# Kernel optimization log

Hardware: AMD Instinct MI355X
Metric: run time of the kernel (lower is better)

## Reference

```python
import jax, jax.numpy as jnp
import numpy as np

B, GRID, CIN, COUT, TDIM, NMODES = 32, 128, 32, 32, 256, 32
M = NMODES // 2 + 1  # kept modes per axis = 17
FFT_NORM = 'forward'


def setup_inputs() -> dict:
    key = jax.random.key(0)
    ks = jax.random.split(key, 10)
    w_std = float(np.sqrt(1.0 / (2.0 * CIN)))          # normal_initializer(in_co_dim)
    k_std = float(np.sqrt(1.0 / TDIM))                 # ~lecun_normal for Dense kernels
    wshape = (M, M, CIN, COUT)
    return {
        'x': jax.random.normal(ks[0], (B, GRID, GRID, CIN), jnp.float32),
        't_emb': jax.random.normal(ks[1], (B, TDIM), jnp.float32),
        'w1_real': w_std * jax.random.normal(ks[2], wshape, jnp.float32),
        'w1_imag': w_std * jax.random.normal(ks[3], wshape, jnp.float32),
        'w2_real': w_std * jax.random.normal(ks[4], wshape, jnp.float32),
        'w2_imag': w_std * jax.random.normal(ks[5], wshape, jnp.float32),
        'k1_real': k_std * jax.random.normal(ks[6], (TDIM, M), jnp.float32),
        'k1_imag': k_std * jax.random.normal(ks[7], (TDIM, M), jnp.float32),
        'k2_real': k_std * jax.random.normal(ks[8], (TDIM, M), jnp.float32),
        'k2_imag': k_std * jax.random.normal(ks[9], (TDIM, M), jnp.float32),
    }


def reference(x, t_emb, w1_real, w1_imag, w2_real, w2_imag,
              k1_real, k1_imag, k2_real, k2_imag):
    b, n = x.shape[0], x.shape[1]
    # rFFT2 over spatial axes: (b, n, n//2+1, cin) complex
    x_ft = jnp.fft.rfft2(x, axes=(1, 2), norm=FFT_NORM)

    w1 = w1_real + 1j * w1_imag  # (M, M, cin, cout)
    w2 = w2_real + 1j * w2_imag
    # Time modulation: Dense(no bias) -> complex per-mode scale t[b, i].
    # The original builds diag(t) and einsums it into the weights; that equals a
    # simple broadcast scale over the first mode axis, fused here.
    t1 = (t_emb @ k1_real) + 1j * (t_emb @ k1_imag)  # (b, M)
    t2 = (t_emb @ k2_real) + 1j * (t_emb @ k2_imag)

    # Mode-truncated complex channel contraction, scaled by t along axis i.
    xf1 = jnp.einsum('bijc,ijco->bijo', x_ft[:, :M, :M, :], w1) * t1[:, :, None, None]
    xf2 = jnp.einsum('bijc,ijco->bijo', x_ft[:, -M:, :M, :], w2) * t2[:, :, None, None]

    out_ft = jnp.zeros((b, n, n // 2 + 1, COUT), dtype=jnp.complex64)
    out_ft = out_ft.at[:, :M, :M, :].set(xf1)
    out_ft = out_ft.at[:, -M:, :M, :].set(xf2)

    return jnp.fft.irfft2(out_ft, s=(n, n), axes=(1, 2), norm=FFT_NORM)
```

## Files before the change

kernel.cpp:

```cpp
#include <hip/hip_runtime.h>
#include <stdint.h>


#define TWO_PI_OVER_128 0.04908738521234052f

__global__ __launch_bounds__(128) void k_tproj(
    const float* __restrict__ temb, const float* __restrict__ k1r, const float* __restrict__ k1i,
    const float* __restrict__ k2r, const float* __restrict__ k2i, float* __restrict__ tbuf)
{
    int b = blockIdx.x, tid = threadIdx.x;
    __shared__ float ts[256];
    for (int d = tid; d < 256; d += 128) ts[d] = temb[b * 256 + d];
    __syncthreads();
    if (tid < 68) {
        int which = (tid >= 34) ? 1 : 0;
        int rem = tid - which * 34;
        int i = rem >> 1, part = rem & 1;
        const float* kp = which ? (part ? k2i : k2r) : (part ? k1i : k1r);
        float a0 = 0.f, a1 = 0.f, a2 = 0.f, a3 = 0.f;
        for (int d = 0; d < 256; d += 4) {
            a0 = fmaf(ts[d],     kp[(d)     * 17 + i], a0);
            a1 = fmaf(ts[d + 1], kp[(d + 1) * 17 + i], a1);
            a2 = fmaf(ts[d + 2], kp[(d + 2) * 17 + i], a2);
            a3 = fmaf(ts[d + 3], kp[(d + 3) * 17 + i], a3);
        }
        tbuf[((which * 32 + b) * 17 + i) * 2 + part] = (a0 + a1) + (a2 + a3);
    }
}

__global__ __launch_bounds__(64) void k_fwd_y(const float* __restrict__ x, float2* __restrict__ T1)
{
    int blk = blockIdx.x;
    int b = blk >> 7, xr = blk & 127;
    __shared__ float xs[128 * 32];
    __shared__ float2 cst[128];
    int tid = threadIdx.x;
    {
        float s0, c0; sincosf(TWO_PI_OVER_128 * (float)tid, &s0, &c0);
        cst[tid] = make_float2(c0, -s0);
        float s1, c1; sincosf(TWO_PI_OVER_128 * (float)(tid + 64), &s1, &c1);
        cst[tid + 64] = make_float2(c1, -s1);
    }
    const float4* xv = (const float4*)(x + ((size_t)blk << 12));
    float4* xs4 = (float4*)xs;
#pragma unroll
    for (int i = 0; i < 16; ++i) xs4[tid + (i << 6)] = xv[tid + (i << 6)];
    __syncthreads();
    for (int i = tid; i < 2016; i += 64) {
        int y = (i >> 5) + 1, c = i & 31;
        float a = xs[(y << 5) + c], q = xs[((128 - y) << 5) + c];
        xs[(y << 5) + c] = a + q;
        xs[((128 - y) << 5) + c] = a - q;
    }
    __syncthreads();
    int jg = tid >> 3, cg = tid & 7, c0 = cg << 2;
    float re[2][4] = {{0,0,0,0},{0,0,0,0}}, im[2][4] = {{0,0,0,0},{0,0,0,0}};
    int j0 = jg, j1 = jg + 8;
    int idx0 = 0, idx1 = 0;
    for (int y = 1; y <= 63; ++y) {
        idx0 = (idx0 + j0) & 127;
        idx1 = (idx1 + j1) & 127;
        float2 w0 = cst[idx0], w1 = cst[idx1];
        float4 s = *(const float4*)&xs[(y << 5) + c0];
        float4 d = *(const float4*)&xs[((128 - y) << 5) + c0];
        re[0][0] = fmaf(s.x, w0.x, re[0][0]);
        re[0][1] = fmaf(s.y, w0.x, re[0][1]);
        re[0][2] = fmaf(s.z, w0.x, re[0][2]);
        re[0][3] = fmaf(s.w, w0.x, re[0][3]);
        im[0][0] = fmaf(d.x, w0.y, im[0][0]);
        im[0][1] = fmaf(d.y, w0.y, im[0][1]);
        im[0][2] = fmaf(d.z, w0.y, im[0][2]);
        im[0][3] = fmaf(d.w, w0.y, im[0][3]);
        re[1][0] = fmaf(s.x, w1.x, re[1][0]);
        re[1][1] = fmaf(s.y, w1.x, re[1][1]);
        re[1][2] = fmaf(s.z, w1.x, re[1][2]);
        re[1][3] = fmaf(s.w, w1.x, re[1][3]);
        im[1][0] = fmaf(d.x, w1.y, im[1][0]);
        im[1][1] = fmaf(d.y, w1.y, im[1][1]);
        im[1][2] = fmaf(d.z, w1.y, im[1][2]);
        im[1][3] = fmaf(d.w, w1.y, im[1][3]);
    }
    const float s_ = 1.f / 16384.f;
    float x0[4], x64[4];
    *(float4*)x0  = *(const float4*)&xs[c0];
    *(float4*)x64 = *(const float4*)&xs[(64 << 5) + c0];
#pragma unroll
    for (int t = 0; t < 2; ++t) {
        int j = jg + t * 8;
        float sg = (j & 1) ? -1.f : 1.f;
        float2* p = T1 + (((size_t)(b * 17 + j) * 128 + xr) << 5) + c0;
        float4 v0 = make_float4((re[t][0] + x0[0] + sg * x64[0]) * s_, im[t][0] * s_,
                                (re[t][1] + x0[1] + sg * x64[1]) * s_, im[t][1] * s_);
        float4 v1 = make_float4((re[t][2] + x0[2] + sg * x64[2]) * s_, im[t][2] * s_,
                                (re[t][3] + x0[3] + sg * x64[3]) * s_, im[t][3] * s_);
        ((float4*)p)[0] = v0; ((float4*)p)[1] = v1;
    }
    {
        float re2[4] = {0,0,0,0}, im2[4] = {0,0,0,0};
        float2 w16 = cst[(16 * (jg + 1)) & 127];
        for (int y = jg + 1; y <= 63; y += 8) {
            float4 s = *(const float4*)&xs[(y << 5) + c0];
            float4 d = *(const float4*)&xs[((128 - y) << 5) + c0];
            re2[0] = fmaf(s.x, w16.x, re2[0]); re2[1] = fmaf(s.y, w16.x, re2[1]);
            re2[2] = fmaf(s.z, w16.x, re2[2]); re2[3] = fmaf(s.w, w16.x, re2[3]);
            im2[0] = fmaf(d.x, w16.y, im2[0]); im2[1] = fmaf(d.y, w16.y, im2[1]);
            im2[2] = fmaf(d.z, w16.y, im2[2]); im2[3] = fmaf(d.w, w16.y, im2[3]);
        }
#pragma unroll
        for (int t = 0; t < 4; ++t) {
            re2[t] += __shfl_xor(re2[t], 8);
            re2[t] += __shfl_xor(re2[t], 16);
            re2[t] += __shfl_xor(re2[t], 32);
            im2[t] += __shfl_xor(im2[t], 8);
            im2[t] += __shfl_xor(im2[t], 16);
            im2[t] += __shfl_xor(im2[t], 32);
        }
        if (jg == 0) {
            float2* p = T1 + (((size_t)(b * 17 + 16) * 128 + xr) << 5) + c0;
            float4 v0 = make_float4((re2[0] + x0[0] + x64[0]) * s_, im2[0] * s_,
                                    (re2[1] + x0[1] + x64[1]) * s_, im2[1] * s_);
            float4 v1 = make_float4((re2[2] + x0[2] + x64[2]) * s_, im2[2] * s_,
                                    (re2[3] + x0[3] + x64[3]) * s_, im2[3] * s_);
            ((float4*)p)[0] = v0; ((float4*)p)[1] = v1;
        }
    }
}

#define XFS 34
__global__ __launch_bounds__(512) void k_mid_fused(
    const float2* __restrict__ T1, const float* __restrict__ w1r, const float* __restrict__ w1i,
    const float* __restrict__ w2r, const float* __restrict__ w2i,
    const float* __restrict__ tbuf, float2* __restrict__ U)
{
    int blk = blockIdx.x;
    int b = blk / 17, j = blk - b * 17;
    __shared__ float4 Ts4[2048];
    __shared__ float2 Xf[34 * XFS];
    __shared__ float2 cst[128];
    int tid = threadIdx.x;
    const float4* s4 = (const float4*)(T1 + (size_t)blk * 4096);
    for (int i = tid; i < 2048; i += 512) Ts4[i] = s4[i];
    if (tid < 128) {
        float s, c; sincosf(TWO_PI_OVER_128 * (float)tid, &s, &c);
        cst[tid] = make_float2(c, s);
    }
    __syncthreads();
    for (int i = tid; i < 1008; i += 512) {
        int xx = (i >> 4) + 1, cp = i & 15;
        float4 a = Ts4[(xx << 4) + cp], q = Ts4[((128 - xx) << 4) + cp];
        Ts4[(xx << 4) + cp] = make_float4(a.x + q.x, a.y + q.y, a.z + q.z, a.w + q.w);
        Ts4[((128 - xx) << 4) + cp] = make_float4(a.x - q.x, a.y - q.y, a.z - q.z, a.w - q.w);
    }
    __syncthreads();
    if (tid < 288) {
        int cp = tid & 15, u = tid >> 4;
        float4 t0 = Ts4[cp], t64 = Ts4[(64 << 4) + cp];
        if (u < 16) {
            int f = u + 1;
            int idx = 0;
            float P0=0,Q0=0,R0=0,T0=0,P1=0,Q1=0,R1=0,T1a=0;
            for (int xx = 1; xx <= 63; ++xx) {
                idx = (idx + f) & 127;
                float2 w = cst[idx];
                float4 S = Ts4[(xx << 4) + cp];
                float4 D = Ts4[((128 - xx) << 4) + cp];
                P0 = fmaf(S.x, w.x, P0); Q0 = fmaf(D.y, w.y, Q0);
                R0 = fmaf(S.y, w.x, R0); T0 = fmaf(D.x, w.y, T0);
                P1 = fmaf(S.z, w.x, P1); Q1 = fmaf(D.w, w.y, Q1);
                R1 = fmaf(S.w, w.x, R1); T1a = fmaf(D.z, w.y, T1a);
            }
            float sg = (f & 1) ? -1.f : 1.f;
            float b0r = t0.x + sg * t64.x, b0i = t0.y + sg * t64.y;
            float b1r = t0.z + sg * t64.z, b1i = t0.w + sg * t64.w;
            int ia = f, ib = 34 - f;
            Xf[ia * XFS + cp*2]   = make_float2(P0 + Q0 + b0r, R0 - T0 + b0i);
            Xf[ia * XFS + cp*2+1] = make_float2(P1 + Q1 + b1r, R1 - T1a + b1i);
            Xf[ib * XFS + cp*2]   = make_float2(P0 - Q0 + b0r, R0 + T0 + b0i);
            Xf[ib * XFS + cp*2+1] = make_float2(P1 - Q1 + b1r, R1 + T1a + b1i);
        } else if (u == 16) {
            float A0=0,B0=0,A1=0,B1=0;
            for (int xx = 1; xx <= 63; ++xx) {
                float4 S = Ts4[(xx << 4) + cp];
                A0 += S.x; B0 += S.y; A1 += S.z; B1 += S.w;
            }
            Xf[cp*2]   = make_float2(A0 + t0.x + t64.x, B0 + t0.y + t64.y);
            Xf[cp*2+1] = make_float2(A1 + t0.z + t64.z, B1 + t0.w + t64.w);
        } else {
            int idx = 0;
            float p0=0,q0=0,r0=0,s0=0,p1=0,q1=0,r1=0,s1=0;
            for (int xx = 1; xx <= 63; ++xx) {
                idx = (idx + 111) & 127;
                float2 w = cst[idx];
                float4 S = Ts4[(xx << 4) + cp];
                float4 D = Ts4[((128 - xx) << 4) + cp];
                p0 = fmaf(S.x, w.x, p0); q0 = fmaf(D.y, w.y, q0);
                r0 = fmaf(S.y, w.x, r0); s0 = fmaf(D.x, w.y, s0);
                p1 = fmaf(S.z, w.x, p1); q1 = fmaf(D.w, w.y, q1);
                r1 = fmaf(S.w, w.x, r1); s1 = fmaf(D.z, w.y, s1);
            }
            float c0r = t0.x - t64.x, c0i = t0.y - t64.y;
            float c1r = t0.z - t64.z, c1i = t0.w - t64.w;
            Xf[17*XFS + cp*2]   = make_float2(p0 + q0 + c0r, r0 - s0 + c0i);
            Xf[17*XFS + cp*2+1] = make_float2(p1 + q1 + c1r, r1 - s1 + c1i);
        }
    }
    __syncthreads();
    float2* Ys = (float2*)Ts4;
    if (tid < 272) {
        int oq = tid & 7, ii = tid >> 3;
        int o0 = oq << 2;
        int irow = (ii < 17) ? ii : ii - 17;
        const float* wr = ((ii < 17) ? w1r : w2r) + ((irow * 17 + j) << 10) + o0;
        const float* wi = ((ii < 17) ? w1i : w2i) + ((irow * 17 + j) << 10) + o0;
        float ar0=0,ai0=0,ar1=0,ai1=0,ar2=0,ai2=0,ar3=0,ai3=0;
#pragma unroll 4
        for (int c = 0; c < 32; ++c) {
            float2 xv = Xf[ii * XFS + c];
            float4 wre = *(const float4*)(wr + (c << 5));
            float4 wim = *(const float4*)(wi + (c << 5));
            ar0 = fmaf(xv.x, wre.x, ar0); ar0 = fmaf(-xv.y, wim.x, ar0);
            ai0 = fmaf(xv.x, wim.x, ai0); ai0 = fmaf( xv.y, wre.x, ai0);
            ar1 = fmaf(xv.x, wre.y, ar1); ar1 = fmaf(-xv.y, wim.y, ar1);
            ai1 = fmaf(xv.x, wim.y, ai1); ai1 = fmaf( xv.y, wre.y, ai1);
            ar2 = fmaf(xv.x, wre.z, ar2); ar2 = fmaf(-xv.y, wim.z, ar2);
            ai2 = fmaf(xv.x, wim.z, ai2); ai2 = fmaf( xv.y, wre.z, ai2);
            ar3 = fmaf(xv.x, wre.w, ar3); ar3 = fmaf(-xv.y, wim.w, ar3);
            ai3 = fmaf(xv.x, wim.w, ai3); ai3 = fmaf( xv.y, wre.w, ai3);
        }
        int which = (ii >= 17) ? 1 : 0;
        const float* tp = tbuf + ((which * 32 + b) * 17 + irow) * 2;
        float tr = tp[0], ti = tp[1];
        float2* yp = Ys + ii * 32 + o0;
        float4 y01 = make_float4(ar0 * tr - ai0 * ti, ar0 * ti + ai0 * tr,
                                 ar1 * tr - ai1 * ti, ar1 * ti + ai1 * tr);
        float4 y23 = make_float4(ar2 * tr - ai2 * ti, ar2 * ti + ai2 * tr,
                                 ar3 * tr - ai3 * ti, ar3 * ti + ai3 * tr);
        ((float4*)yp)[0] = y01;
        ((float4*)yp)[1] = y23;
    }
    __syncthreads();
    {
        int o = tid & 31, g = tid >> 5;
        float yr[34], yi[34];
#pragma unroll
        for (int i = 0; i < 34; ++i) { float2 v = Ys[i * 32 + o]; yr[i] = v.x; yi[i] = v.y; }
        float2* Ub = U + ((size_t)b * 128 * 17 + j) * 32 + o;
        if (g == 0) {
            float sr = 0.f, si = 0.f;
#pragma unroll
            for (int i = 0; i < 34; ++i) { sr += yr[i]; si += yi[i]; }
            Ub[0] = make_float2(sr, si);
        }
        if (g == 1) {
            float sr = 0.f, si = 0.f;
#pragma unroll
            for (int i = 0; i < 34; ++i) {
                float sg2 = (i & 1) ? -1.f : 1.f;
                sr = fmaf(sg2, yr[i], sr); si = fmaf(sg2, yi[i], si);
            }
            Ub[(size_t)64 * 544] = make_float2(sr, si);
        }
        for (int k = 0; k < 2; ++k) {
            int x = 1 + g + (k << 4);
            float A1e=0,A1o=0,A2e=0,A2o=0,A3e=0,A3o=0,A4e=0,A4o=0;
            int idx = 0;
#pragma unroll
            for (int i = 0; i < 17; ++i) {
                float2 w = cst[idx];
                if (i & 1) {
                    A1o = fmaf(yr[i], w.x, A1o); A4o = fmaf(yr[i], w.y, A4o);
                    A3o = fmaf(yi[i], w.x, A3o); A2o = fmaf(yi[i], w.y, A2o);
                } else {
                    A1e = fmaf(yr[i], w.x, A1e); A4e = fmaf(yr[i], w.y, A4e);
                    A3e = fmaf(yi[i], w.x, A3e); A2e = fmaf(yi[i], w.y, A2e);
                }
                idx = (idx + x) & 127;
            }
            idx = (111 * x) & 127;
#pragma unroll
            for (int i = 17; i < 34; ++i) {
                float2 w = cst[idx];
                if (i & 1) {
                    A1o = fmaf(yr[i], w.x, A1o); A4o = fmaf(yr[i], w.y, A4o);
                    A3o = fmaf(yi[i], w.x, A3o); A2o = fmaf(yi[i], w.y, A2o);
                } else {
                    A1e = fmaf(yr[i], w.x, A1e); A4e = fmaf(yr[i], w.y, A4e);
                    A3e = fmaf(yi[i], w.x, A3e); A2e = fmaf(yi[i], w.y, A2e);
                }
                idx = (idx + x) & 127;
            }
            float A1 = A1e + A1o, A2 = A2e + A2o, A3 = A3e + A3o, A4 = A4e + A4o;
            float E1 = A1e - A1o, E2 = A2o - A2e, E3 = A3e - A3o, E4 = A4o - A4e;
            Ub[(size_t)x * 544]         = make_float2(A1 - A2, A3 + A4);
            Ub[(size_t)(128 - x) * 544] = make_float2(A1 + A2, A3 - A4);
            Ub[(size_t)(64 - x) * 544]  = make_float2(E1 - E2, E3 + E4);
            Ub[(size_t)(64 + x) * 544]  = make_float2(E1 + E2, E3 - E4);
        }
    }
}

__global__ __launch_bounds__(256) void k_fwd_x_mix(
    const float2* __restrict__ T1, const float* __restrict__ w1r, const float* __restrict__ w1i,
    const float* __restrict__ w2r, const float* __restrict__ w2i,
    const float* __restrict__ tbuf, float2* __restrict__ Y)
{
    int blk = blockIdx.x;
    int b = blk / 17, j = blk - b * 17;
    __shared__ float4 Ts4[2048];
    __shared__ float2 Xf[34 * 32];
    int tid = threadIdx.x;
    const float4* s4 = (const float4*)(T1 + (size_t)blk * 4096);
    for (int i = tid; i < 2048; i += 256) Ts4[i] = s4[i];
    __syncthreads();
    {
        int cp = tid & 15, g = tid >> 4;
        int il[3] = {g, g + 16, g + 32};
        float stc[3], sts[3];
#pragma unroll
        for (int t = 0; t < 3; ++t) {
            int i = il[t];
            int f = (i < 17) ? i : i + 94;
            float a = -TWO_PI_OVER_128 * (float)(f & 127);
            sincosf(a, &sts[t], &stc[t]);
        }
        float cr[3] = {1.f, 1.f, 1.f}, ci[3] = {0.f, 0.f, 0.f};
        float r0[3] = {0,0,0}, i0[3] = {0,0,0}, r1[3] = {0,0,0}, i1[3] = {0,0,0};
        const float4* Tc = Ts4 + cp;
#pragma unroll 2
        for (int xx = 0; xx < 128; ++xx) {
            float4 tv = Tc[xx << 4];
#pragma unroll
            for (int t = 0; t < 3; ++t) {
                r0[t] += tv.x * cr[t] - tv.y * ci[t];
                i0[t] += tv.x * ci[t] + tv.y * cr[t];
                r1[t] += tv.z * cr[t] - tv.w * ci[t];
                i1[t] += tv.z * ci[t] + tv.w * cr[t];
                float nr = cr[t] * stc[t] - ci[t] * sts[t];
                ci[t] = fmaf(cr[t], sts[t], ci[t] * stc[t]);
                cr[t] = nr;
            }
        }
#pragma unroll
        for (int t = 0; t < 3; ++t) {
            int i = il[t];
            if (i < 34) {
                Xf[i * 32 + cp * 2]     = make_float2(r0[t], i0[t]);
                Xf[i * 32 + cp * 2 + 1] = make_float2(r1[t], i1[t]);
            }
        }
    }
    __syncthreads();
    {
        int o = tid & 31, gi = tid >> 5;
#pragma unroll
        for (int t = 0; t < 5; ++t) {
            int ii = gi + (t << 3);
            if (ii < 34) {
                int irow = (ii < 17) ? ii : ii - 17;
                const float* wr = ((ii < 17) ? w1r : w2r) + ((irow * 17 + j) << 10) + o;
                const float* wi = ((ii < 17) ? w1i : w2i) + ((irow * 17 + j) << 10) + o;
                float ar = 0.f, ai = 0.f;
#pragma unroll 8
                for (int cc2 = 0; cc2 < 32; ++cc2) {
                    float2 xv = Xf[ii * 32 + cc2];
                    float wre = wr[cc2 << 5];
                    float wim = wi[cc2 << 5];
                    ar += xv.x * wre - xv.y * wim;
                    ai += xv.x * wim + xv.y * wre;
                }
                int which = (ii >= 17) ? 1 : 0;
                const float* tp = tbuf + ((which * 32 + b) * 17 + irow) * 2;
                float tr = tp[0], ti = tp[1];
                Y[(size_t)blk * (34 * 32) + ii * 32 + o] =
                    make_float2(ar * tr - ai * ti, ar * ti + ai * tr);
            }
        }
    }
}

__global__ __launch_bounds__(256) void k_inv_x(const float2* __restrict__ Y, float2* __restrict__ U)
{
    int blk = blockIdx.x;
    int b = blk / 17, j = blk - b * 17;
    __shared__ float2 Ys[34 * 32];
    __shared__ float ct[128], st[128];
    int tid = threadIdx.x;
    if (tid < 128) {
        float a = TWO_PI_OVER_128 * (float)tid;
        sincosf(a, &st[tid], &ct[tid]);
    }
    const float2* src = Y + (size_t)blk * (34 * 32);
    for (int i = tid; i < 34 * 32; i += 256) Ys[i] = src[i];
    __syncthreads();
    int o = tid & 31, g = tid >> 5;
    float yr[34], yi[34];
#pragma unroll
    for (int i = 0; i < 34; ++i) { float2 v = Ys[i * 32 + o]; yr[i] = v.x; yi[i] = v.y; }
    for (int xi = 0; xi < 16; ++xi) {
        int xr = (xi << 3) + g;
        float cx = ct[xr], sx = st[xr];
        float cr = 1.f, ci = 0.f, re = 0.f, im = 0.f;
#pragma unroll
        for (int i = 0; i < 17; ++i) {
            re += yr[i] * cr - yi[i] * ci;
            im += yr[i] * ci + yi[i] * cr;
            float nr = cr * cx - ci * sx;
            ci = fmaf(cr, sx, ci * cx);
            cr = nr;
        }
        int k2 = (111 * xr) & 127;
        cr = ct[k2]; ci = st[k2];
#pragma unroll
        for (int i = 17; i < 34; ++i) {
            re += yr[i] * cr - yi[i] * ci;
            im += yr[i] * ci + yi[i] * cr;
            float nr = cr * cx - ci * sx;
            ci = fmaf(cr, sx, ci * cx);
            cr = nr;
        }
        U[(((size_t)(b * 128 + xr)) * 17 + j) * 32 + o] = make_float2(re, im);
    }
}

__global__ __launch_bounds__(128) void k_inv_y(const float2* __restrict__ U, float* __restrict__ out)
{
    int blk = blockIdx.x;
    __shared__ float2 Us[17 * 32];
    __shared__ float2 cst[128];
    int tid = threadIdx.x;
    {
        float s, c; sincosf(TWO_PI_OVER_128 * (float)tid, &s, &c);
        cst[tid] = make_float2(c, s);
    }
    const float4* src4 = (const float4*)(U + (size_t)blk * 544);
    float4* Us4 = (float4*)Us;
    for (int i = tid; i < 272; i += 128) Us4[i] = src4[i];
    __syncthreads();
    int cg = tid & 15, yg = tid >> 4, c0 = cg << 1;
    float base0, base1;
    {
        float4 v = *(const float4*)&Us[c0];
        base0 = v.x; base1 = v.z;
    }
    float urr[16][2], uii[16][2];
#pragma unroll
    for (int jj = 1; jj <= 16; ++jj) {
        float4 v = *(const float4*)&Us[jj * 32 + c0];
        urr[jj-1][0] = 2.f * v.x; uii[jj-1][0] = 2.f * v.y;
        urr[jj-1][1] = 2.f * v.z; uii[jj-1][1] = 2.f * v.w;
    }
    float* op = out + ((size_t)blk << 12);
    for (int k = 0; k < 4; ++k) {
        int y = 1 + yg + (k << 3);
        float Ae0=0,Ao0=0,Be0=0,Bo0=0,Ae1=0,Ao1=0,Be1=0,Bo1=0;
        int idx = y;
#pragma unroll
        for (int jj = 0; jj < 16; ++jj) {
            float2 w = cst[idx];
            if (jj & 1) {
                Ae0 = fmaf(urr[jj][0], w.x, Ae0); Be0 = fmaf(uii[jj][0], w.y, Be0);
                Ae1 = fmaf(urr[jj][1], w.x, Ae1); Be1 = fmaf(uii[jj][1], w.y, Be1);
            } else {
                Ao0 = fmaf(urr[jj][0], w.x, Ao0); Bo0 = fmaf(uii[jj][0], w.y, Bo0);
                Ao1 = fmaf(urr[jj][1], w.x, Ao1); Bo1 = fmaf(uii[jj][1], w.y, Bo1);
            }
            idx = (idx + y) & 127;
        }
        float s0 = Ae0 + Ao0, d0 = Be0 + Bo0, e0 = Ae0 - Ao0, f0 = Be0 - Bo0;
        float s1 = Ae1 + Ao1, d1 = Be1 + Bo1, e1 = Ae1 - Ao1, f1 = Be1 - Bo1;
        *(float2*)&op[(y << 5) + c0]         = make_float2(base0 + s0 - d0, base1 + s1 - d1);
        *(float2*)&op[((128 - y) << 5) + c0] = make_float2(base0 + s0 + d0, base1 + s1 + d1);
        *(float2*)&op[((64 - y) << 5) + c0]  = make_float2(base0 + e0 + f0, base1 + e1 + f1);
        *(float2*)&op[((64 + y) << 5) + c0]  = make_float2(base0 + e0 - f0, base1 + e1 - f1);
    }
    if (yg == 0) {
        float s0 = 0.f, s1 = 0.f, a0 = 0.f, a1 = 0.f;
#pragma unroll
        for (int jj = 0; jj < 16; ++jj) {
            s0 += urr[jj][0]; s1 += urr[jj][1];
            float sg = (jj & 1) ? 1.f : -1.f;
            a0 = fmaf(sg, urr[jj][0], a0); a1 = fmaf(sg, urr[jj][1], a1);
        }
        *(float2*)&op[c0]             = make_float2(base0 + s0, base1 + s1);
        *(float2*)&op[(64 << 5) + c0] = make_float2(base0 + a0, base1 + a1);
    }
}

extern "C" void kernel_launch(void* const* d_in, const int* in_sizes, int n_in,
                              void* d_out, int out_size, void* d_ws, size_t ws_size,
                              hipStream_t stream)
{
    const float* x    = (const float*)d_in[0];
    const float* temb = (const float*)d_in[1];
    const float* w1r  = (const float*)d_in[2];
    const float* w1i  = (const float*)d_in[3];
    const float* w2r  = (const float*)d_in[4];
    const float* w2i  = (const float*)d_in[5];
    const float* k1r  = (const float*)d_in[6];
    const float* k1i  = (const float*)d_in[7];
    const float* k2r  = (const float*)d_in[8];
    const float* k2i  = (const float*)d_in[9];
    float* out = (float*)d_out;

    char* ws = (char*)d_ws;
    const size_t T1_BYTES = 17825792;
    const size_t NEED_FUSED = 2 * T1_BYTES + 8704;

    if (ws_size >= NEED_FUSED) {
        float2* T1 = (float2*)ws;
        float2* U  = (float2*)(ws + T1_BYTES);
        float*  tb = (float*)(ws + 2 * T1_BYTES);
        k_tproj    <<<32,   128, 0, stream>>>(temb, k1r, k1i, k2r, k2i, tb);
        k_fwd_y    <<<4096, 64,  0, stream>>>(x, T1);
        k_mid_fused<<<544,  512, 0, stream>>>(T1, w1r, w1i, w2r, w2i, tb, U);
        k_inv_y    <<<4096, 128, 0, stream>>>(U, out);
    } else {
        float2* T1 = (float2*)ws;
        float2* Yb = (float2*)(ws + T1_BYTES);
        float*  tb = (float*)(ws + T1_BYTES + 4734976);
        float2* U  = T1;
        k_tproj    <<<32,   128, 0, stream>>>(temb, k1r, k1i, k2r, k2i, tb);
        k_fwd_y    <<<4096, 64,  0, stream>>>(x, T1);
        k_fwd_x_mix<<<544,  256, 0, stream>>>(T1, w1r, w1i, w2r, w2i, tb, Yb);
        k_inv_x    <<<544,  256, 0, stream>>>(Yb, U);
        k_inv_y    <<<4096, 128, 0, stream>>>(U, out);
    }
}
```

Baseline: 187.6 us.

## Add second radix-2 folding to forward DFTs and fuse time projection into mid kernel

The forward y-axis and x-axis DFT stages gain an extra even/odd symmetry fold around the quarter point, which halves the inner DFT loop length from 63 to 31 iterations. Row 32 and row 96 are handled as separate terms. The time-embedding projection kernel is removed, and its dot products now run inside spare threads of the fused mid kernel, saving one launch and a global round trip. This adds index arithmetic and more complex fold logic, and every mid block now recomputes the projection redundantly.

```diff
diff --git a/kernel.cpp b/kernel.cpp
--- a/kernel.cpp
+++ b/kernel.cpp
@@ -3,6 +3,13 @@
 
 
 #define TWO_PI_OVER_128 0.04908738521234052f
+
+__device__ __forceinline__ float4 f4add(float4 a, float4 b) {
+    return make_float4(a.x + b.x, a.y + b.y, a.z + b.z, a.w + b.w);
+}
+__device__ __forceinline__ float4 f4sub(float4 a, float4 b) {
+    return make_float4(a.x - b.x, a.y - b.y, a.z - b.z, a.w - b.w);
+}
 
 __global__ __launch_bounds__(128) void k_tproj(
     const float* __restrict__ temb, const float* __restrict__ k1r, const float* __restrict__ k1i,
@@ -46,23 +53,37 @@
 #pragma unroll
     for (int i = 0; i < 16; ++i) xs4[tid + (i << 6)] = xv[tid + (i << 6)];
     __syncthreads();
-    for (int i = tid; i < 2016; i += 64) {
-        int y = (i >> 5) + 1, c = i & 31;
-        float a = xs[(y << 5) + c], q = xs[((128 - y) << 5) + c];
-        xs[(y << 5) + c] = a + q;
-        xs[((128 - y) << 5) + c] = a - q;
+    for (int i = tid; i < 1024; i += 64) {
+        int c = i & 31, t = i >> 5;
+        if (t < 31) {
+            int y = t + 1;
+            float a  = xs[(y << 5) + c],        bb = xs[((64 - y) << 5) + c];
+            float cc = xs[((64 + y) << 5) + c], d  = xs[((128 - y) << 5) + c];
+            float Sy = a + d, Dy = a - d, Sm = bb + cc, Dm = bb - cc;
+            xs[(y << 5) + c]         = Sy + Sm;
+            xs[((64 - y) << 5) + c]  = Sy - Sm;
+            xs[((128 - y) << 5) + c] = Dy - Dm;
+            xs[((64 + y) << 5) + c]  = Dy + Dm;
+        } else {
+            float a = xs[(32 << 5) + c], q = xs[(96 << 5) + c];
+            xs[(32 << 5) + c] = a + q;
+            xs[(96 << 5) + c] = a - q;
+        }
     }
     __syncthreads();
     int jg = tid >> 3, cg = tid & 7, c0 = cg << 2;
+    int p = jg & 1;
     float re[2][4] = {{0,0,0,0},{0,0,0,0}}, im[2][4] = {{0,0,0,0},{0,0,0,0}};
     int j0 = jg, j1 = jg + 8;
     int idx0 = 0, idx1 = 0;
-    for (int y = 1; y <= 63; ++y) {
+    for (int y = 1; y <= 31; ++y) {
         idx0 = (idx0 + j0) & 127;
         idx1 = (idx1 + j1) & 127;
         float2 w0 = cst[idx0], w1 = cst[idx1];
-        float4 s = *(const float4*)&xs[(y << 5) + c0];
-        float4 d = *(const float4*)&xs[((128 - y) << 5) + c0];
+        int sr = p ? (64 - y) : y;
+        int dr = p ? (64 + y) : (128 - y);
+        float4 s = *(const float4*)&xs[(sr << 5) + c0];
+        float4 d = *(const float4*)&xs[(dr << 5) + c0];
         re[0][0] = fmaf(s.x, w0.x, re[0][0]);
         re[0][1] = fmaf(s.y, w0.x, re[0][1]);
         re[0][2] = fmaf(s.z, w0.x, re[0][2]);
@@ -81,24 +102,31 @@
         im[1][3] = fmaf(d.w, w1.y, im[1][3]);
     }
     const float s_ = 1.f / 16384.f;
-    float x0[4], x64[4];
-    *(float4*)x0  = *(const float4*)&xs[c0];
-    *(float4*)x64 = *(const float4*)&xs[(64 << 5) + c0];
+    float x0[4], x64[4], S32v[4], D32v[4];
+    *(float4*)x0   = *(const float4*)&xs[c0];
+    *(float4*)x64  = *(const float4*)&xs[(64 << 5) + c0];
+    *(float4*)S32v = *(const float4*)&xs[(32 << 5) + c0];
+    *(float4*)D32v = *(const float4*)&xs[(96 << 5) + c0];
+    float2 w32 = cst[(j0 << 5) & 127];
+    float sg = p ? -1.f : 1.f;
 #pragma unroll
     for (int t = 0; t < 2; ++t) {
         int j = jg + t * 8;
-        float sg = (j & 1) ? -1.f : 1.f;
-        float2* p = T1 + (((size_t)(b * 17 + j) * 128 + xr) << 5) + c0;
-        float4 v0 = make_float4((re[t][0] + x0[0] + sg * x64[0]) * s_, im[t][0] * s_,
-                                (re[t][1] + x0[1] + sg * x64[1]) * s_, im[t][1] * s_);
-        float4 v1 = make_float4((re[t][2] + x0[2] + sg * x64[2]) * s_, im[t][2] * s_,
-                                (re[t][3] + x0[3] + sg * x64[3]) * s_, im[t][3] * s_);
-        ((float4*)p)[0] = v0; ((float4*)p)[1] = v1;
+        float2* pp = T1 + (((size_t)(b * 17 + j) * 128 + xr) << 5) + c0;
+        float4 v0 = make_float4((re[t][0] + x0[0] + sg * x64[0] + S32v[0] * w32.x) * s_,
+                                (im[t][0] + D32v[0] * w32.y) * s_,
+                                (re[t][1] + x0[1] + sg * x64[1] + S32v[1] * w32.x) * s_,
+                                (im[t][1] + D32v[1] * w32.y) * s_);
+        float4 v1 = make_float4((re[t][2] + x0[2] + sg * x64[2] + S32v[2] * w32.x) * s_,
+                                (im[t][2] + D32v[2] * w32.y) * s_,
+                                (re[t][3] + x0[3] + sg * x64[3] + S32v[3] * w32.x) * s_,
+                                (im[t][3] + D32v[3] * w32.y) * s_);
+        ((float4*)pp)[0] = v0; ((float4*)pp)[1] = v1;
     }
     {
         float re2[4] = {0,0,0,0}, im2[4] = {0,0,0,0};
         float2 w16 = cst[(16 * (jg + 1)) & 127];
-        for (int y = jg + 1; y <= 63; y += 8) {
+        for (int y = jg + 1; y <= 31; y += 8) {
             float4 s = *(const float4*)&xs[(y << 5) + c0];
             float4 d = *(const float4*)&xs[((128 - y) << 5) + c0];
             re2[0] = fmaf(s.x, w16.x, re2[0]); re2[1] = fmaf(s.y, w16.x, re2[1]);
@@ -116,12 +144,12 @@
             im2[t] += __shfl_xor(im2[t], 32);
         }
         if (jg == 0) {
-            float2* p = T1 + (((size_t)(b * 17 + 16) * 128 + xr) << 5) + c0;
-            float4 v0 = make_float4((re2[0] + x0[0] + x64[0]) * s_, im2[0] * s_,
-                                    (re2[1] + x0[1] + x64[1]) * s_, im2[1] * s_);
-            float4 v1 = make_float4((re2[2] + x0[2] + x64[2]) * s_, im2[2] * s_,
-                                    (re2[3] + x0[3] + x64[3]) * s_, im2[3] * s_);
-            ((float4*)p)[0] = v0; ((float4*)p)[1] = v1;
+            float2* pp = T1 + (((size_t)(b * 17 + 16) * 128 + xr) << 5) + c0;
+            float4 v0 = make_float4((re2[0] + x0[0] + x64[0] + S32v[0]) * s_, im2[0] * s_,
+                                    (re2[1] + x0[1] + x64[1] + S32v[1]) * s_, im2[1] * s_);
+            float4 v1 = make_float4((re2[2] + x0[2] + x64[2] + S32v[2]) * s_, im2[2] * s_,
+                                    (re2[3] + x0[3] + x64[3] + S32v[3]) * s_, im2[3] * s_);
+            ((float4*)pp)[0] = v0; ((float4*)pp)[1] = v1;
         }
     }
 }
@@ -130,13 +158,15 @@
 __global__ __launch_bounds__(512) void k_mid_fused(
     const float2* __restrict__ T1, const float* __restrict__ w1r, const float* __restrict__ w1i,
     const float* __restrict__ w2r, const float* __restrict__ w2i,
-    const float* __restrict__ tbuf, float2* __restrict__ U)
+    const float* __restrict__ temb, const float* __restrict__ k1r, const float* __restrict__ k1i,
+    const float* __restrict__ k2r, const float* __restrict__ k2i, float2* __restrict__ U)
 {
     int blk = blockIdx.x;
     int b = blk / 17, j = blk - b * 17;
     __shared__ float4 Ts4[2048];
     __shared__ float2 Xf[34 * XFS];
     __shared__ float2 cst[128];
+    __shared__ float tl[68];
     int tid = threadIdx.x;
     const float4* s4 = (const float4*)(T1 + (size_t)blk * 4096);
     for (int i = tid; i < 2048; i += 512) Ts4[i] = s4[i];
@@ -145,64 +175,76 @@
         cst[tid] = make_float2(c, s);
     }
     __syncthreads();
-    for (int i = tid; i < 1008; i += 512) {
-        int xx = (i >> 4) + 1, cp = i & 15;
-        float4 a = Ts4[(xx << 4) + cp], q = Ts4[((128 - xx) << 4) + cp];
-        Ts4[(xx << 4) + cp] = make_float4(a.x + q.x, a.y + q.y, a.z + q.z, a.w + q.w);
-        Ts4[((128 - xx) << 4) + cp] = make_float4(a.x - q.x, a.y - q.y, a.z - q.z, a.w - q.w);
+    {
+        int t = tid >> 4, cp = tid & 15;
+        if (t < 31) {
+            int y = t + 1;
+            float4 a  = Ts4[(y << 4) + cp],        bb = Ts4[((64 - y) << 4) + cp];
+            float4 cc = Ts4[((64 + y) << 4) + cp], d  = Ts4[((128 - y) << 4) + cp];
+            float4 Sy = f4add(a, d), Dy = f4sub(a, d);
+            float4 Sm = f4add(bb, cc), Dm = f4sub(bb, cc);
+            Ts4[(y << 4) + cp]         = f4add(Sy, Sm);
+            Ts4[((64 - y) << 4) + cp]  = f4sub(Sy, Sm);
+            Ts4[((128 - y) << 4) + cp] = f4sub(Dy, Dm);
+            Ts4[((64 + y) << 4) + cp]  = f4add(Dy, Dm);
+        } else {
+            float4 a = Ts4[(32 << 4) + cp], q = Ts4[(96 << 4) + cp];
+            Ts4[(32 << 4) + cp] = f4add(a, q);
+            Ts4[(96 << 4) + cp] = f4sub(a, q);
+        }
     }
     __syncthreads();
     if (tid < 288) {
         int cp = tid & 15, u = tid >> 4;
+        int f = (u < 16) ? (u + 1) : ((u == 16) ? 0 : 111);
+        int p = f & 1;
         float4 t0 = Ts4[cp], t64 = Ts4[(64 << 4) + cp];
+        float P0=0,Q0=0,R0=0,T0=0,P1=0,Q1=0,R1=0,T1a=0;
+        int idx = 0;
+        for (int xx = 1; xx <= 31; ++xx) {
+            idx = (idx + f) & 127;
+            float2 w = cst[idx];
+            float4 S = Ts4[((p ? (64 - xx) : xx) << 4) + cp];
+            float4 D = Ts4[((p ? (64 + xx) : (128 - xx)) << 4) + cp];
+            P0 = fmaf(S.x, w.x, P0); Q0 = fmaf(D.y, w.y, Q0);
+            R0 = fmaf(S.y, w.x, R0); T0 = fmaf(D.x, w.y, T0);
+            P1 = fmaf(S.z, w.x, P1); Q1 = fmaf(D.w, w.y, Q1);
+            R1 = fmaf(S.w, w.x, R1); T1a = fmaf(D.z, w.y, T1a);
+        }
+        {
+            float2 w32 = cst[(f << 5) & 127];
+            float4 S32 = Ts4[(32 << 4) + cp], D32 = Ts4[(96 << 4) + cp];
+            P0 = fmaf(S32.x, w32.x, P0); Q0 = fmaf(D32.y, w32.y, Q0);
+            R0 = fmaf(S32.y, w32.x, R0); T0 = fmaf(D32.x, w32.y, T0);
+            P1 = fmaf(S32.z, w32.x, P1); Q1 = fmaf(D32.w, w32.y, Q1);
+            R1 = fmaf(S32.w, w32.x, R1); T1a = fmaf(D32.z, w32.y, T1a);
+        }
+        float sg = p ? -1.f : 1.f;
+        float b0r = t0.x + sg * t64.x, b0i = t0.y + sg * t64.y;
+        float b1r = t0.z + sg * t64.z, b1i = t0.w + sg * t64.w;
+        int ia = (u == 16) ? 0 : ((u == 17) ? 17 : f);
+        Xf[ia * XFS + cp*2]   = make_float2(P0 + Q0 + b0r, R0 - T0 + b0i);
+        Xf[ia * XFS + cp*2+1] = make_float2(P1 + Q1 + b1r, R1 - T1a + b1i);
         if (u < 16) {
-            int f = u + 1;
-            int idx = 0;
-            float P0=0,Q0=0,R0=0,T0=0,P1=0,Q1=0,R1=0,T1a=0;
-            for (int xx = 1; xx <= 63; ++xx) {
-                idx = (idx + f) & 127;
-                float2 w = cst[idx];
-                float4 S = Ts4[(xx << 4) + cp];
-                float4 D = Ts4[((128 - xx) << 4) + cp];
-                P0 = fmaf(S.x, w.x, P0); Q0 = fmaf(D.y, w.y, Q0);
-                R0 = fmaf(S.y, w.x, R0); T0 = fmaf(D.x, w.y, T0);
-                P1 = fmaf(S.z, w.x, P1); Q1 = fmaf(D.w, w.y, Q1);
-                R1 = fmaf(S.w, w.x, R1); T1a = fmaf(D.z, w.y, T1a);
-            }
-            float sg = (f & 1) ? -1.f : 1.f;
-            float b0r = t0.x + sg * t64.x, b0i = t0.y + sg * t64.y;
-            float b1r = t0.z + sg * t64.z, b1i = t0.w + sg * t64.w;
-            int ia = f, ib = 34 - f;
-            Xf[ia * XFS + cp*2]   = make_float2(P0 + Q0 + b0r, R0 - T0 + b0i);
-            Xf[ia * XFS + cp*2+1] = make_float2(P1 + Q1 + b1r, R1 - T1a + b1i);
+            int ib = 34 - f;
             Xf[ib * XFS + cp*2]   = make_float2(P0 - Q0 + b0r, R0 + T0 + b0i);
             Xf[ib * XFS + cp*2+1] = make_float2(P1 - Q1 + b1r, R1 + T1a + b1i);
-        } else if (u == 16) {
-            float A0=0,B0=0,A1=0,B1=0;
-            for (int xx = 1; xx <= 63; ++xx) {
-                float4 S = Ts4[(xx << 4) + cp];
-                A0 += S.x; B0 += S.y; A1 += S.z; B1 += S.w;
-            }
-            Xf[cp*2]   = make_float2(A0 + t0.x + t64.x, B0 + t0.y + t64.y);
-            Xf[cp*2+1] = make_float2(A1 + t0.z + t64.z, B1 + t0.w + t64.w);
-        } else {
-            int idx = 0;
-            float p0=0,q0=0,r0=0,s0=0,p1=0,q1=0,r1=0,s1=0;
-            for (int xx = 1; xx <= 63; ++xx) {
-                idx = (idx + 111) & 127;
-                float2 w = cst[idx];
-                float4 S = Ts4[(xx << 4) + cp];
-                float4 D = Ts4[((128 - xx) << 4) + cp];
-                p0 = fmaf(S.x, w.x, p0); q0 = fmaf(D.y, w.y, q0);
-                r0 = fmaf(S.y, w.x, r0); s0 = fmaf(D.x, w.y, s0);
-                p1 = fmaf(S.z, w.x, p1); q1 = fmaf(D.w, w.y, q1);
-                r1 = fmaf(S.w, w.x, r1); s1 = fmaf(D.z, w.y, s1);
-            }
-            float c0r = t0.x - t64.x, c0i = t0.y - t64.y;
-            float c1r = t0.z - t64.z, c1i = t0.w - t64.w;
-            Xf[17*XFS + cp*2]   = make_float2(p0 + q0 + c0r, r0 - s0 + c0i);
-            Xf[17*XFS + cp*2+1] = make_float2(p1 + q1 + c1r, r1 - s1 + c1i);
-        }
+        }
+    } else if (tid >= 320 && tid < 388) {
+        int r = tid - 320;
+        int which = (r >= 34) ? 1 : 0;
+        int rem = r - which * 34;
+        int i = rem >> 1, part = rem & 1;
+        const float* kp = which ? (part ? k2i : k2r) : (part ? k1i : k1r);
+        const float* tb = temb + b * 256;
+        float a0 = 0.f, a1 = 0.f, a2 = 0.f, a3 = 0.f;
+        for (int d = 0; d < 256; d += 4) {
+            a0 = fmaf(tb[d],     kp[(d)     * 17 + i], a0);
+            a1 = fmaf(tb[d + 1], kp[(d + 1) * 17 + i], a1);
+            a2 = fmaf(tb[d + 2], kp[(d + 2) * 17 + i], a2);
+            a3 = fmaf(tb[d + 3], kp[(d + 3) * 17 + i], a3);
+        }
+        tl[which * 34 + (i << 1) + part] = (a0 + a1) + (a2 + a3);
     }
     __syncthreads();
     float2* Ys = (float2*)Ts4;
@@ -228,8 +270,7 @@
             ai3 = fmaf(xv.x, wim.w, ai3); ai3 = fmaf( xv.y, wre.w, ai3);
         }
         int which = (ii >= 17) ? 1 : 0;
-        const float* tp = tbuf + ((which * 32 + b) * 17 + irow) * 2;
-        float tr = tp[0], ti = tp[1];
+        float tr = tl[which * 34 + (irow << 1)], ti = tl[which * 34 + (irow << 1) + 1];
         float2* yp = Ys + ii * 32 + o0;
         float4 y01 = make_float4(ar0 * tr - ai0 * ti, ar0 * ti + ai0 * tr,
                                  ar1 * tr - ai1 * ti, ar1 * ti + ai1 * tr);
@@ -509,10 +550,9 @@
     if (ws_size >= NEED_FUSED) {
         float2* T1 = (float2*)ws;
         float2* U  = (float2*)(ws + T1_BYTES);
-        float*  tb = (float*)(ws + 2 * T1_BYTES);
-        k_tproj    <<<32,   128, 0, stream>>>(temb, k1r, k1i, k2r, k2i, tb);
         k_fwd_y    <<<4096, 64,  0, stream>>>(x, T1);
-        k_mid_fused<<<544,  512, 0, stream>>>(T1, w1r, w1i, w2r, w2i, tb, U);
+        k_mid_fused<<<544,  512, 0, stream>>>(T1, w1r, w1i, w2r, w2i,
+                                              temb, k1r, k1i, k2r, k2i, U);
         k_inv_y    <<<4096, 128, 0, stream>>>(U, out);
     } else {
         float2* T1 = (float2*)ws;
```

Result: faster. 183.1 us (median of 2 runs) (-2.4%).
